# Optimization experiments

Measured on AMD Instinct MI355X. Metric: run time of the kernel, lower is better.

## Reference

```python
import jax, jax.numpy as jnp
import numpy as np

NEG_SLOPE = 0.2


def add_self_loops(edge_index, num_nodes):
    loop = jnp.arange(num_nodes, dtype=edge_index.dtype)
    return jnp.concatenate([edge_index, jnp.stack([loop, loop])], axis=1)


def gat_conv(x, edge_index, W, att_src, att_dst, bias, heads, out_ch, concat):
    # x: [N, F_in]; edge_index: [2, E]; W: [F_in, heads*out_ch]
    # att_src/att_dst: [heads, out_ch]; bias: [heads*out_ch] or [out_ch]
    N = x.shape[0]
    ei = add_self_loops(edge_index, N)
    src, dst = ei[0], ei[1]
    xw = (x @ W).reshape(N, heads, out_ch)          # [N, H, C]
    a_src = jnp.einsum('nhc,hc->nh', xw, att_src)    # [N, H]
    a_dst = jnp.einsum('nhc,hc->nh', xw, att_dst)    # [N, H]
    e = a_src[src] + a_dst[dst]                      # [E', H]
    e = jax.nn.leaky_relu(e, NEG_SLOPE)
    # segment softmax over edges grouped by destination node
    e_max = jax.ops.segment_max(e, dst, num_segments=N)  # [N, H]
    e_exp = jnp.exp(e - e_max[dst])
    denom = jax.ops.segment_sum(e_exp, dst, num_segments=N)  # [N, H]
    alpha = e_exp / denom[dst]                       # [E', H]
    msg = xw[src] * alpha[:, :, None]                # [E', H, C]
    out = jax.ops.segment_sum(msg, dst, num_segments=N)  # [N, H, C]
    if concat:
        out = out.reshape(N, heads * out_ch)
    else:
        out = out.mean(axis=1)
    return out + bias


def setup_inputs() -> dict:
    key = jax.random.key(0)
    ks = jax.random.split(key, 10)
    N, E = 100000, 1600000
    F_in, hid, heads, F_out = 128, 32, 4, 40
    s = 0.1
    x = jax.random.normal(ks[0], (N, F_in), dtype=jnp.float32)
    edge_index = jax.random.randint(ks[1], (2, E), 0, N, dtype=jnp.int64)
    W1 = jax.random.normal(ks[2], (F_in, heads * hid), dtype=jnp.float32) * s
    att_src1 = jax.random.normal(ks[3], (heads, hid), dtype=jnp.float32) * s
    att_dst1 = jax.random.normal(ks[4], (heads, hid), dtype=jnp.float32) * s
    b1 = jax.random.normal(ks[5], (heads * hid,), dtype=jnp.float32) * s
    W2 = jax.random.normal(ks[6], (heads * hid, F_out), dtype=jnp.float32) * s
    att_src2 = jax.random.normal(ks[7], (1, F_out), dtype=jnp.float32) * s
    att_dst2 = jax.random.normal(ks[8], (1, F_out), dtype=jnp.float32) * s
    b2 = jax.random.normal(ks[9], (F_out,), dtype=jnp.float32) * s
    return {"x": x, "edge_index": edge_index, "W1": W1, "att_src1": att_src1,
            "att_dst1": att_dst1, "b1": b1, "W2": W2, "att_src2": att_src2,
            "att_dst2": att_dst2, "b2": b2}


def reference(x, edge_index, W1, att_src1, att_dst1, b1, W2, att_src2, att_dst2, b2):
    h = gat_conv(x, edge_index, W1, att_src1, att_dst1, b1, heads=4, out_ch=32, concat=True)
    h = jax.nn.relu(h)
    out = gat_conv(h, edge_index, W2, att_src2, att_dst2, b2, heads=1, out_ch=40, concat=True)
    return out
```

## Files before the change

### kernel.cpp

```cpp
#include <hip/hip_runtime.h>
#include <hip/hip_bf16.h>

#define NEG_SLOPE 0.2f
#define LOG2E 1.4426950408889634f
#define HWREG_XCC_ID_FULL (((32 - 1) << 11) | (0 << 6) | 20)

typedef _Float16 f16;
typedef f16 f16x8 __attribute__((ext_vector_type(8)));
typedef float f32x4 __attribute__((ext_vector_type(4)));

__device__ __forceinline__ unsigned pack_h2(float a, float b) {
    union { f16 h[2]; unsigned u; } c;
    c.h[0] = (f16)a; c.h[1] = (f16)b;
    return c.u;
}

__device__ __forceinline__ void load_edge(const void* ei, int f64, int e, int E, int& s, int& d) {
    if (f64) {
        const long long* p = (const long long*)ei;
        s = (int)p[e];
        d = (int)p[(long long)E + e];
    } else {
        const int* p = (const int*)ei;
        s = p[e];
        d = p[E + e];
    }
}

__global__ void k_init(const int* __restrict__ ei32, int npairs, int* __restrict__ flag,
                       const float* __restrict__ W1, const float* __restrict__ W2,
                       f16* __restrict__ W1t, f16* __restrict__ W2t,
                       uint4* __restrict__ deg_part4, int nzero) {
    const int b = blockIdx.x, t = threadIdx.x;
    if (b == 0) {
        __shared__ int found;
        if (t == 0) found = 0;
        __syncthreads();
        for (int i = t; i < npairs; i += 256) {
            if (ei32[2 * i + 1] != 0) found = 1;
        }
        __syncthreads();
        if (t == 0) *flag = found ? 0 : 1;
    } else if (b <= 88) {
        int o = (b - 1) * 256 + t;
        if (o < 128 * 128) {
            int n = o >> 7, k = o & 127;
            W1t[o] = (f16)W1[k * 128 + n];
        } else {
            int o2 = o - 128 * 128;
            if (o2 < 48 * 128) {
                int n = o2 >> 7, k = o2 & 127;
                W2t[o2] = (f16)(n < 40 ? W2[k * 40 + n] : 0.f);
            }
        }
    } else {
        int idx = (b - 89) * 256 + t;
        if (idx < nzero) deg_part4[idx] = (uint4){0, 0, 0, 0};
    }
}

__global__ void k_degree(const void* __restrict__ ei, const int* __restrict__ flag,
                         int* __restrict__ deg_part, int* __restrict__ rank, int N, int E) {
    int e = blockIdx.x * blockDim.x + threadIdx.x;
    if (e >= E) return;
    int d;
    if (*flag) d = (int)((const long long*)ei)[(long long)E + e];
    else       d = ((const int*)ei)[E + e];
    int xcc = (int)(__builtin_amdgcn_s_getreg(HWREG_XCC_ID_FULL) & 7u);
    int lr = atomicAdd(&deg_part[xcc * N + d], 1);
    rank[e] = (xcc << 24) | lr;
}

__global__ __launch_bounds__(1024) void k_scan_blk(int* __restrict__ deg_part,
                                                   int* __restrict__ offsets,
                                                   int* __restrict__ blksum, int N) {
    __shared__ int wsums[16];
    const int t = threadIdx.x;
    const int lane = t & 63;
    const int wid = t >> 6;
    int idx = blockIdx.x * 4096 + t * 4;
    int v0 = 0, v1 = 0, v2 = 0, v3 = 0;
    if (((N & 3) == 0) && (idx + 3 < N)) {
        uint4 u[8];
#pragma unroll
        for (int x = 0; x < 8; x++) u[x] = *(uint4*)&deg_part[x * N + idx];
        int p0 = 0, p1 = 0, p2 = 0, p3 = 0;
#pragma unroll
        for (int x = 0; x < 8; x++) {
            uint4 w = u[x];
            u[x] = (uint4){(unsigned)p0, (unsigned)p1, (unsigned)p2, (unsigned)p3};
            p0 += (int)w.x; p1 += (int)w.y; p2 += (int)w.z; p3 += (int)w.w;
        }
#pragma unroll
        for (int x = 0; x < 8; x++) *(uint4*)&deg_part[x * N + idx] = u[x];
        v0 = p0; v1 = p1; v2 = p2; v3 = p3;
    } else if (idx < N) {
        int vv[4] = {0, 0, 0, 0};
        for (int i = 0; i < 4; i++) {
            int d = idx + i;
            if (d >= N) break;
            int p = 0;
#pragma unroll
            for (int x = 0; x < 8; x++) {
                int t0 = deg_part[x * N + d];
                deg_part[x * N + d] = p;
                p += t0;
            }
            vv[i] = p;
        }
        v0 = vv[0]; v1 = vv[1]; v2 = vv[2]; v3 = vv[3];
    }
    int s1 = v0 + v1, s2 = s1 + v2, s3 = s2 + v3;
    int inc = s3;
#pragma unroll
    for (int off = 1; off < 64; off <<= 1) {
        int y = __shfl_up(inc, off);
        if (lane >= off) inc += y;
    }
    if (lane == 63) wsums[wid] = inc;
    __syncthreads();
    if (wid == 0) {
        int v = (lane < 16) ? wsums[lane] : 0;
        int wi = v;
#pragma unroll
        for (int off = 1; off < 16; off <<= 1) {
            int y = __shfl_up(wi, off);
            if (lane >= off) wi += y;
        }
        if (lane < 16) wsums[lane] = wi - v;
        if (lane == 15) blksum[blockIdx.x] = wi;
    }
    __syncthreads();
    int excl = wsums[wid] + (inc - s3);
    if (idx + 0 < N) offsets[idx + 1] = excl + v0;
    if (idx + 1 < N) offsets[idx + 2] = excl + s1;
    if (idx + 2 < N) offsets[idx + 3] = excl + s2;
    if (idx + 3 < N) offsets[idx + 4] = excl + s3;
}

__global__ void k_scan_top(const int* __restrict__ blksum, int* __restrict__ blkoff, int G) {
    int l = threadIdx.x;
    int v = (l < G) ? blksum[l] : 0;
    int inc = v;
#pragma unroll
    for (int off = 1; off < 64; off <<= 1) {
        int y = __shfl_up(inc, off);
        if (l >= off) inc += y;
    }
    if (l < G) blkoff[l] = inc - v;
}

__global__ void k_scan_add(int* __restrict__ offsets, const int* __restrict__ blkoff, int N) {
    int n = blockIdx.x * blockDim.x + threadIdx.x;
    if (n >= N) return;
    offsets[n + 1] += blkoff[n >> 12];
    if (n == 0) offsets[0] = 0;
}

__global__ void k_scatter(const void* __restrict__ ei, const int* __restrict__ flag,
                          const int* __restrict__ offsets, const int* __restrict__ deg_part,
                          const int* __restrict__ rank, int* __restrict__ csr_src,
                          int N, int E) {
    int e = blockIdx.x * blockDim.x + threadIdx.x;
    if (e >= E) return;
    int s, d;
    load_edge(ei, *flag, e, E, s, d);
    int r = rank[e];
    int xcc = r >> 24;
    int lr = r & 0xFFFFFF;
    csr_src[offsets[d] + deg_part[xcc * N + d] + lr] = s;
}

__global__ __launch_bounds__(256) void k_gemm1(const float* __restrict__ X,
                                               const f16* __restrict__ W1t,
                                               const float* __restrict__ as1,
                                               const float* __restrict__ ad1,
                                               f16* __restrict__ Afh,
                                               float* __restrict__ aS1,
                                               float* __restrict__ aD1, int N) {
    __shared__ f16 sA[64 * 136];
    __shared__ f16 sB[128 * 136];
    const int t = threadIdx.x;
    const int row0 = blockIdx.x * 64;

    {
        int r = t >> 2, seg = t & 3;
        int row = row0 + r;
        if (row >= N) row = N - 1;
        const float4* xg = (const float4*)(X + (size_t)row * 128 + seg * 32);
        unsigned tmp[16];
#pragma unroll
        for (int j = 0; j < 8; j++) {
            float4 v = xg[j];
            tmp[2 * j]     = pack_h2(v.x, v.y);
            tmp[2 * j + 1] = pack_h2(v.z, v.w);
        }
        uint4* dst = (uint4*)&sA[r * 136 + seg * 32];
#pragma unroll
        for (int j = 0; j < 4; j++) dst[j] = ((uint4*)tmp)[j];
        int n = t >> 1, half = (t & 1) * 64;
        const uint4* src = (const uint4*)(W1t + n * 128 + half);
        uint4* dw = (uint4*)&sB[n * 136 + half];
#pragma unroll
        for (int j = 0; j < 8; j++) dw[j] = src[j];
    }
    __syncthreads();

    const int w = t >> 6, lane = t & 63, ln = lane & 15, q = lane >> 4;
    f32x4 acc[8];
#pragma unroll
    for (int c = 0; c < 8; c++) acc[c] = (f32x4){0.f, 0.f, 0.f, 0.f};

#pragma unroll
    for (int ks = 0; ks < 4; ks++) {
        f16x8 a = *(const f16x8*)&sA[(w * 16 + ln) * 136 + ks * 32 + q * 8];
#pragma unroll
        for (int c = 0; c < 8; c++) {
            f16x8 b = *(const f16x8*)&sB[(c * 16 + ln) * 136 + ks * 32 + q * 8];
            acc[c] = __builtin_amdgcn_mfma_f32_16x16x32_f16(a, b, acc[c], 0, 0, 0);
        }
    }

    const size_t H64 = (size_t)N * 64;
#pragma unroll
    for (int c = 0; c < 8; c++) {
        int half = c >> 2, cc = c & 3;
#pragma unroll
        for (int reg = 0; reg < 4; reg++) {
            int rg = row0 + w * 16 + q * 4 + reg;
            if (rg < N) Afh[half * H64 + (size_t)rg * 64 + cc * 16 + ln] = (f16)acc[c][reg];
        }
    }

    float ps[4][4], pd[4][4];
#pragma unroll
    for (int h = 0; h < 4; h++) {
        float as_lo = as1[32 * h + ln], as_hi = as1[32 * h + 16 + ln];
        float ad_lo = ad1[32 * h + ln], ad_hi = ad1[32 * h + 16 + ln];
#pragma unroll
        for (int reg = 0; reg < 4; reg++) {
            ps[h][reg] = acc[2 * h][reg] * as_lo + acc[2 * h + 1][reg] * as_hi;
            pd[h][reg] = acc[2 * h][reg] * ad_lo + acc[2 * h + 1][reg] * ad_hi;
        }
    }
#pragma unroll
    for (int h = 0; h < 4; h++)
#pragma unroll
        for (int reg = 0; reg < 4; reg++)
#pragma unroll
            for (int off = 1; off < 16; off <<= 1) {
                ps[h][reg] += __shfl_xor(ps[h][reg], off);
                pd[h][reg] += __shfl_xor(pd[h][reg], off);
            }
#pragma unroll
    for (int h = 0; h < 4; h++) {
        if (ln == 2 * h) {
#pragma unroll
            for (int reg = 0; reg < 4; reg++) {
                int rg = row0 + w * 16 + q * 4 + reg;
                if (rg < N) aS1[rg * 4 + h] = ps[h][reg] * LOG2E;
            }
        }
        if (ln == 2 * h + 1) {
#pragma unroll
            for (int reg = 0; reg < 4; reg++) {
                int rg = row0 + w * 16 + q * 4 + reg;
                if (rg < N) aD1[rg * 4 + h] = pd[h][reg] * LOG2E;
            }
        }
    }
}

__global__ __launch_bounds__(256) void k_gemm2(const f16* __restrict__ Hfh,
                                               const f16* __restrict__ W2t,
                                               const float* __restrict__ as2,
                                               const float* __restrict__ ad2,
                                               f16* __restrict__ X2f,
                                               float* __restrict__ aS2,
                                               float* __restrict__ aD2, int N) {
    __shared__ f16 sA[64 * 136];
    __shared__ f16 sB[48 * 136];
    const int t = threadIdx.x;
    const int row0 = blockIdx.x * 64;
    const size_t H64 = (size_t)N * 64;
    {
        int r = t >> 2, seg = t & 3;
        int row = row0 + r;
        if (row >= N) row = N - 1;
        const uint4* hg = (const uint4*)(Hfh + (size_t)(seg >> 1) * H64 +
                                         (size_t)row * 64 + (seg & 1) * 32);
        uint4* dst = (uint4*)&sA[r * 136 + seg * 32];
#pragma unroll
        for (int j = 0; j < 4; j++) dst[j] = hg[j];
        const uint4* wsrc = (const uint4*)W2t;
#pragma unroll
        for (int u = t; u < 768; u += 256) {
            int o = u * 8;
            int n = o >> 7, ko = o & 127;
            *(uint4*)&sB[n * 136 + ko] = wsrc[u];
        }
    }
    __syncthreads();

    const int w = t >> 6, lane = t & 63, ln = lane & 15, q = lane >> 4;
    f32x4 acc[3];
#pragma unroll
    for (int c = 0; c < 3; c++) acc[c] = (f32x4){0.f, 0.f, 0.f, 0.f};

#pragma unroll
    for (int ks = 0; ks < 4; ks++) {
        f16x8 a = *(const f16x8*)&sA[(w * 16 + ln) * 136 + ks * 32 + q * 8];
#pragma unroll
        for (int c = 0; c < 3; c++) {
            f16x8 b = *(const f16x8*)&sB[(c * 16 + ln) * 136 + ks * 32 + q * 8];
            acc[c] = __builtin_amdgcn_mfma_f32_16x16x32_f16(a, b, acc[c], 0, 0, 0);
        }
    }

#pragma unroll
    for (int c = 0; c < 3; c++) {
        int col = c * 16 + ln;
        if (col < 40) {
#pragma unroll
            for (int reg = 0; reg < 4; reg++) {
                int rg = row0 + w * 16 + q * 4 + reg;
                if (rg < N) X2f[(size_t)rg * 64 + col] = (f16)acc[c][reg];
            }
        }
    }

    float ps[4], pd[4];
#pragma unroll
    for (int reg = 0; reg < 4; reg++) { ps[reg] = 0.f; pd[reg] = 0.f; }
#pragma unroll
    for (int c = 0; c < 3; c++) {
        int col = c * 16 + ln;
        float as_ = (col < 40) ? as2[col] : 0.f;
        float ad_ = (col < 40) ? ad2[col] : 0.f;
#pragma unroll
        for (int reg = 0; reg < 4; reg++) {
            ps[reg] = fmaf(acc[c][reg], as_, ps[reg]);
            pd[reg] = fmaf(acc[c][reg], ad_, pd[reg]);
        }
    }
#pragma unroll
    for (int reg = 0; reg < 4; reg++) {
#pragma unroll
        for (int off = 1; off < 16; off <<= 1) {
            ps[reg] += __shfl_xor(ps[reg], off);
            pd[reg] += __shfl_xor(pd[reg], off);
        }
        int rg = row0 + w * 16 + q * 4 + reg;
        if (rg < N) {
            if (ln == 0) aS2[rg] = ps[reg] * LOG2E;
            if (ln == 1) aD2[rg] = pd[reg] * LOG2E;
        }
    }
}

__global__ __launch_bounds__(128) void k_msg1(const int* __restrict__ offsets,
                                              const int* __restrict__ csr_src,
                                              const float* __restrict__ aS,
                                              const float* __restrict__ aD,
                                              const f16* __restrict__ Afh,
                                              const float* __restrict__ b1,
                                              f16* __restrict__ Hfh, int N, int NB) {
    const int lane = threadIdx.x & 63;
    const int pass = (blockIdx.x >= NB) ? 1 : 0;
    const int blk = blockIdx.x - pass * NB;
    const int n = blk * 2 + (threadIdx.x >> 6);
    const bool node_ok = (n < N);
    const int g = lane >> 3;
    const int p = lane & 7;
    const int h = pass * 2 + (p >> 2);
    const size_t H64 = (size_t)N * 64;
    const f16* Af = Afh + (size_t)pass * H64;

    int b = 0, e = 0;
    float adh = 0.f;
    if (node_ok) {
        b = offsets[n];
        e = offsets[n + 1];
        adh = aD[n * 4 + h];
    }

    float acc[8];
#pragma unroll
    for (int k = 0; k < 8; k++) acc[k] = 0.f;
    float wsum = 0.f;

    if (node_ok) {
        float xs = aS[n * 4 + h] + adh;
        float ws = __builtin_amdgcn_exp2f(fmaxf(xs, NEG_SLOPE * xs));
        if (g != 0) ws = 0.f;
        const f16x8 hv = *(const f16x8*)(Af + (size_t)n * 64 + p * 8);
#pragma unroll
        for (int k = 0; k < 8; k++) acc[k] = fmaf(ws, (float)hv[k], acc[k]);
        wsum = ws;
    }

    int sreg = 0;
    if (node_ok && e > b) {
        int idx = b + lane;
        if (idx >= e) idx = e - 1;
        sreg = csr_src[idx];
    }

    int i = b;
#pragma unroll 2
    for (; i < e && (i - b) + 8 <= 64; i += 8) {
        int j = i + g;
        bool valid = (j < e);
        int s = __builtin_amdgcn_ds_bpermute((j - b) << 2, sreg);
        if (!valid) s = 0;
        float sv = aS[s * 4 + h];
        const f16x8 hv = *(const f16x8*)(Af + (size_t)s * 64 + p * 8);
        float x = sv + adh;
        float wgt = __builtin_amdgcn_exp2f(fmaxf(x, NEG_SLOPE * x));
        if (!valid) wgt = 0.f;
#pragma unroll
        for (int k = 0; k < 8; k++) acc[k] = fmaf(wgt, (float)hv[k], acc[k]);
        wsum += wgt;
    }
    for (; i < e; i += 8) {
        int j = i + g;
        bool valid = (j < e);
        int jc = valid ? j : (e - 1);
        int s = csr_src[jc];
        if (!valid) s = 0;
        float sv = aS[s * 4 + h];
        const f16x8 hv = *(const f16x8*)(Af + (size_t)s * 64 + p * 8);
        float x = sv + adh;
        float wgt = __builtin_amdgcn_exp2f(fmaxf(x, NEG_SLOPE * x));
        if (!valid) wgt = 0.f;
#pragma unroll
        for (int k = 0; k < 8; k++) acc[k] = fmaf(wgt, (float)hv[k], acc[k]);
        wsum += wgt;
    }

#pragma unroll
    for (int k = 0; k < 8; k++) {
        acc[k] += __shfl_xor(acc[k], 8);
        acc[k] += __shfl_xor(acc[k], 16);
        acc[k] += __shfl_xor(acc[k], 32);
    }
    wsum += __shfl_xor(wsum, 8);
    wsum += __shfl_xor(wsum, 16);
    wsum += __shfl_xor(wsum, 32);

    if (node_ok && g == 0) {
        float inv = __builtin_amdgcn_rcpf(wsum);
        const float4* bb = (const float4*)(b1 + pass * 64 + p * 8);
        float4 b0 = bb[0], b4 = bb[1];
        float bv[8] = {b0.x, b0.y, b0.z, b0.w, b4.x, b4.y, b4.z, b4.w};
        union { f16 h8[8]; uint4 u; } o;
#pragma unroll
        for (int k = 0; k < 8; k++) {
            float v = fmaf(acc[k], inv, bv[k]);
            o.h8[k] = (f16)fmaxf(v, 0.f);
        }
        *(uint4*)(Hfh + (size_t)pass * H64 + (size_t)n * 64 + p * 8) = o.u;
    }
}

__global__ __launch_bounds__(128) void k_msg2(const int* __restrict__ offsets,
                                              const int* __restrict__ csr_src,
                                              const float* __restrict__ aS,
                                              const float* __restrict__ aD,
                                              const f16* __restrict__ X2f,
                                              const float* __restrict__ b2,
                                              float* __restrict__ OUT, int N) {
    __shared__ float red[2][60][9];
    const int lane = threadIdx.x & 63;
    const int wv = threadIdx.x >> 6;
    const int n = blockIdx.x * 2 + wv;
    const bool node_ok = (n < N);
    const int g = lane / 5;
    const int p = lane % 5;
    const bool lane_ok = (g < 12);

    int b = 0, e = 0;
    float adh = 0.f;
    if (node_ok) {
        b = offsets[n];
        e = offsets[n + 1];
        adh = aD[n];
    }

    float acc[8];
#pragma unroll
    for (int k = 0; k < 8; k++) acc[k] = 0.f;
    float wsum = 0.f;

    if (node_ok) {
        float xs = aS[n] + adh;
        float ws = __builtin_amdgcn_exp2f(fmaxf(xs, NEG_SLOPE * xs));
        if (!(lane_ok && g == 0)) ws = 0.f;
        const f16x8 hv = *(const f16x8*)(X2f + (size_t)n * 64 + p * 8);
#pragma unroll
        for (int k = 0; k < 8; k++) acc[k] = fmaf(ws, (float)hv[k], acc[k]);
        wsum = ws;
    }

    int sreg = 0;
    if (node_ok && e > b) {
        int idx = b + lane;
        if (idx >= e) idx = e - 1;
        sreg = csr_src[idx];
    }

    int i = b;
    for (; i < e && (i - b) + 12 <= 64; i += 12) {
        int j = i + g;
        bool valid = lane_ok && (j < e);
        int s = __builtin_amdgcn_ds_bpermute(((j - b) & 63) << 2, sreg);
        if (!valid) s = 0;
        float sv = aS[s];
        const f16x8 hv = *(const f16x8*)(X2f + (size_t)s * 64 + p * 8);
        float x = sv + adh;
        float wgt = __builtin_amdgcn_exp2f(fmaxf(x, NEG_SLOPE * x));
        if (!valid) wgt = 0.f;
#pragma unroll
        for (int k = 0; k < 8; k++) acc[k] = fmaf(wgt, (float)hv[k], acc[k]);
        wsum += wgt;
    }
    for (; i < e; i += 12) {
        int j = i + g;
        bool valid = lane_ok && (j < e);
        int jc = (j < e) ? j : (e - 1);
        int s = csr_src[jc];
        if (!valid) s = 0;
        float sv = aS[s];
        const f16x8 hv = *(const f16x8*)(X2f + (size_t)s * 64 + p * 8);
        float x = sv + adh;
        float wgt = __builtin_amdgcn_exp2f(fmaxf(x, NEG_SLOPE * x));
        if (!valid) wgt = 0.f;
#pragma unroll
        for (int k = 0; k < 8; k++) acc[k] = fmaf(wgt, (float)hv[k], acc[k]);
        wsum += wgt;
    }

    if (lane_ok) {
#pragma unroll
        for (int k = 0; k < 8; k++) red[wv][lane][k] = acc[k];
        red[wv][lane][8] = wsum;
    }
    __syncthreads();

    if (node_ok && lane < 40) {
        int pp = lane >> 3, kk = lane & 7;
        float s_ = 0.f, ws_ = 0.f;
#pragma unroll
        for (int gg = 0; gg < 12; gg++) {
            s_  += red[wv][gg * 5 + pp][kk];
            ws_ += red[wv][gg * 5][8];
        }
        float inv = __builtin_amdgcn_rcpf(ws_);
        OUT[(size_t)n * 40 + lane] = fmaf(s_, inv, b2[lane]);
    }
}

extern "C" void kernel_launch(void* const* d_in, const int* in_sizes, int n_in,
                              void* d_out, int out_size, void* d_ws, size_t ws_size,
                              hipStream_t stream) {
    const float* x   = (const float*)d_in[0];
    const void*  ei  = d_in[1];
    const float* W1  = (const float*)d_in[2];
    const float* as1 = (const float*)d_in[3];
    const float* ad1 = (const float*)d_in[4];
    const float* b1  = (const float*)d_in[5];
    const float* W2  = (const float*)d_in[6];
    const float* as2 = (const float*)d_in[7];
    const float* ad2 = (const float*)d_in[8];
    const float* b2  = (const float*)d_in[9];
    float* out = (float*)d_out;

    const int N = in_sizes[0] / 128;
    const int E = in_sizes[1] / 2;

    char* w = (char*)d_ws;
    auto alloc = [&](size_t bytes) {
        char* p = w;
        w += (bytes + 15) & ~(size_t)15;
        return p;
    };
    int* flag      = (int*)alloc(16);
    int* offsets   = (int*)alloc((size_t)(N + 1) * 4);
    int* deg_part  = (int*)alloc((size_t)N * 8 * 4);
    int* rank      = (int*)alloc((size_t)E * 4);
    int* csr_src   = (int*)alloc((size_t)E * 4);
    int* blksum    = (int*)alloc(64 * 4);
    int* blkoff    = (int*)alloc(64 * 4);
    float* aS1     = (float*)alloc((size_t)N * 4 * 4);
    float* aD1     = (float*)alloc((size_t)N * 4 * 4);
    float* aS2     = (float*)alloc((size_t)N * 4);
    float* aD2     = (float*)alloc((size_t)N * 4);
    f16* W1t       = (f16*)alloc(128 * 128 * 2);
    f16* W2t       = (f16*)alloc(48 * 128 * 2);
    f16* Afh       = (f16*)alloc((size_t)N * 128 * 2);
    f16* X2f       = (f16*)alloc((size_t)N * 64 * 2);
    f16* Hfh       = (f16*)alloc((size_t)N * 128 * 2);

    const int nzero = 2 * N;
    k_init<<<89 + (nzero + 255) / 256, 256, 0, stream>>>(
        (const int*)ei, 1024, flag, W1, W2, W1t, W2t, (uint4*)deg_part, nzero);

    k_degree<<<(E + 255) / 256, 256, 0, stream>>>(ei, flag, deg_part, rank, N, E);
    const int G = (N + 4095) / 4096;
    k_scan_blk<<<G, 1024, 0, stream>>>(deg_part, offsets, blksum, N);
    k_scan_top<<<1, 64, 0, stream>>>(blksum, blkoff, G);
    k_scan_add<<<(N + 255) / 256, 256, 0, stream>>>(offsets, blkoff, N);
    k_scatter<<<(E + 255) / 256, 256, 0, stream>>>(ei, flag, offsets, deg_part, rank,
                                                   csr_src, N, E);

    const int gb = (N + 63) / 64;
    k_gemm1<<<gb, 256, 0, stream>>>(x, W1t, as1, ad1, Afh, aS1, aD1, N);
    const int NB = (N + 1) / 2;
    k_msg1<<<2 * NB, 128, 0, stream>>>(offsets, csr_src, aS1, aD1, Afh, b1, Hfh, N, NB);

    k_gemm2<<<gb, 256, 0, stream>>>(Hfh, W2t, as2, ad2, X2f, aS2, aD2, N);
    k_msg2<<<(N + 1) / 2, 128, 0, stream>>>(offsets, csr_src, aS2, aD2, X2f, b2, out, N);
}
```

Baseline: 405.3 us.

## Merge split-head layer-1 layout into one pass, add nontemporal loads and stores

Layer-1 features were stored as two half-head planes, and the layer-1 aggregation ran as two passes over the edges. They are now stored as one 128-wide row per node and aggregated in a single pass: 16 lanes cover a row, and each wave handles 4 edges per step instead of 8. This halves the CSR index and attention traversal for layer 1 but doubles the gather width per edge. Nontemporal load and store hints are also added across many streaming accesses, and the message kernels now use 4 waves (256 threads) per block instead of 2. Marking accesses as nontemporal risks evicting data from cache that is later reused, such as Af and Hf, which are read again by the next kernel.

After: 431.4 us. +6.4%, slower.

```diff
diff --git a/kernel.cpp b/kernel.cpp
--- a/kernel.cpp
+++ b/kernel.cpp
@@ -8,23 +8,31 @@
 typedef _Float16 f16;
 typedef f16 f16x8 __attribute__((ext_vector_type(8)));
 typedef float f32x4 __attribute__((ext_vector_type(4)));
+typedef float fvec4 __attribute__((ext_vector_type(4)));
+typedef unsigned uvec4 __attribute__((ext_vector_type(4)));
+
+template <typename T>
+__device__ __forceinline__ T ntload(const T* p) { return __builtin_nontemporal_load(p); }
+template <typename T>
+__device__ __forceinline__ void ntstore(T* p, T v) { __builtin_nontemporal_store(v, p); }
+
+__device__ __forceinline__ float4 ntload4f(const float4* p) {
+    fvec4 v = __builtin_nontemporal_load((const fvec4*)p);
+    return make_float4(v.x, v.y, v.z, v.w);
+}
+__device__ __forceinline__ uint4 ntload4u(const uint4* p) {
+    uvec4 v = __builtin_nontemporal_load((const uvec4*)p);
+    return (uint4){v.x, v.y, v.z, v.w};
+}
+__device__ __forceinline__ void ntstore4u(uint4* p, uint4 v) {
+    uvec4 t = {v.x, v.y, v.z, v.w};
+    __builtin_nontemporal_store(t, (uvec4*)p);
+}
 
 __device__ __forceinline__ unsigned pack_h2(float a, float b) {
     union { f16 h[2]; unsigned u; } c;
     c.h[0] = (f16)a; c.h[1] = (f16)b;
     return c.u;
-}
-
-__device__ __forceinline__ void load_edge(const void* ei, int f64, int e, int E, int& s, int& d) {
-    if (f64) {
-        const long long* p = (const long long*)ei;
-        s = (int)p[e];
-        d = (int)p[(long long)E + e];
-    } else {
-        const int* p = (const int*)ei;
-        s = p[e];
-        d = p[E + e];
-    }
 }
 
 __global__ void k_init(const int* __restrict__ ei32, int npairs, int* __restrict__ flag,
@@ -64,11 +72,11 @@
     int e = blockIdx.x * blockDim.x + threadIdx.x;
     if (e >= E) return;
     int d;
-    if (*flag) d = (int)((const long long*)ei)[(long long)E + e];
-    else       d = ((const int*)ei)[E + e];
+    if (*flag) d = (int)ntload(&((const long long*)ei)[(long long)E + e]);
+    else       d = ntload(&((const int*)ei)[E + e]);
     int xcc = (int)(__builtin_amdgcn_s_getreg(HWREG_XCC_ID_FULL) & 7u);
     int lr = atomicAdd(&deg_part[xcc * N + d], 1);
-    rank[e] = (xcc << 24) | lr;
+    ntstore(&rank[e], (xcc << 24) | lr);
 }
 
 __global__ __launch_bounds__(1024) void k_scan_blk(int* __restrict__ deg_part,
@@ -164,18 +172,26 @@
     int e = blockIdx.x * blockDim.x + threadIdx.x;
     if (e >= E) return;
     int s, d;
-    load_edge(ei, *flag, e, E, s, d);
-    int r = rank[e];
+    if (*flag) {
+        const long long* p = (const long long*)ei;
+        s = (int)ntload(&p[e]);
+        d = (int)ntload(&p[(long long)E + e]);
+    } else {
+        const int* p = (const int*)ei;
+        s = ntload(&p[e]);
+        d = ntload(&p[E + e]);
+    }
+    int r = ntload(&rank[e]);
     int xcc = r >> 24;
     int lr = r & 0xFFFFFF;
-    csr_src[offsets[d] + deg_part[xcc * N + d] + lr] = s;
+    ntstore(&csr_src[offsets[d] + deg_part[xcc * N + d] + lr], s);
 }
 
 __global__ __launch_bounds__(256) void k_gemm1(const float* __restrict__ X,
                                                const f16* __restrict__ W1t,
                                                const float* __restrict__ as1,
                                                const float* __restrict__ ad1,
-                                               f16* __restrict__ Afh,
+                                               f16* __restrict__ Af,
                                                float* __restrict__ aS1,
                                                float* __restrict__ aD1, int N) {
     __shared__ f16 sA[64 * 136];
@@ -191,7 +207,7 @@
         unsigned tmp[16];
 #pragma unroll
         for (int j = 0; j < 8; j++) {
-            float4 v = xg[j];
+            float4 v = ntload4f(&xg[j]);
             tmp[2 * j]     = pack_h2(v.x, v.y);
             tmp[2 * j + 1] = pack_h2(v.z, v.w);
         }
@@ -221,16 +237,13 @@
         }
     }
 
-    const size_t H64 = (size_t)N * 64;
-#pragma unroll
-    for (int c = 0; c < 8; c++) {
-        int half = c >> 2, cc = c & 3;
+#pragma unroll
+    for (int c = 0; c < 8; c++)
 #pragma unroll
         for (int reg = 0; reg < 4; reg++) {
             int rg = row0 + w * 16 + q * 4 + reg;
-            if (rg < N) Afh[half * H64 + (size_t)rg * 64 + cc * 16 + ln] = (f16)acc[c][reg];
-        }
-    }
+            if (rg < N) ntstore(&Af[(size_t)rg * 128 + c * 16 + ln], (f16)acc[c][reg]);
+        }
 
     float ps[4][4], pd[4][4];
 #pragma unroll
@@ -271,7 +284,7 @@
     }
 }
 
-__global__ __launch_bounds__(256) void k_gemm2(const f16* __restrict__ Hfh,
+__global__ __launch_bounds__(256) void k_gemm2(const f16* __restrict__ Hf,
                                                const f16* __restrict__ W2t,
                                                const float* __restrict__ as2,
                                                const float* __restrict__ ad2,
@@ -282,16 +295,14 @@
     __shared__ f16 sB[48 * 136];
     const int t = threadIdx.x;
     const int row0 = blockIdx.x * 64;
-    const size_t H64 = (size_t)N * 64;
     {
         int r = t >> 2, seg = t & 3;
         int row = row0 + r;
         if (row >= N) row = N - 1;
-        const uint4* hg = (const uint4*)(Hfh + (size_t)(seg >> 1) * H64 +
-                                         (size_t)row * 64 + (seg & 1) * 32);
+        const uint4* hg = (const uint4*)(Hf + (size_t)row * 128 + seg * 32);
         uint4* dst = (uint4*)&sA[r * 136 + seg * 32];
 #pragma unroll
-        for (int j = 0; j < 4; j++) dst[j] = hg[j];
+        for (int j = 0; j < 4; j++) dst[j] = ntload4u(&hg[j]);
         const uint4* wsrc = (const uint4*)W2t;
 #pragma unroll
         for (int u = t; u < 768; u += 256) {
@@ -358,23 +369,19 @@
     }
 }
 
-__global__ __launch_bounds__(128) void k_msg1(const int* __restrict__ offsets,
+__global__ __launch_bounds__(256) void k_msg1(const int* __restrict__ offsets,
                                               const int* __restrict__ csr_src,
                                               const float* __restrict__ aS,
                                               const float* __restrict__ aD,
-                                              const f16* __restrict__ Afh,
+                                              const f16* __restrict__ Af,
                                               const float* __restrict__ b1,
-                                              f16* __restrict__ Hfh, int N, int NB) {
+                                              f16* __restrict__ Hf, int N) {
     const int lane = threadIdx.x & 63;
-    const int pass = (blockIdx.x >= NB) ? 1 : 0;
-    const int blk = blockIdx.x - pass * NB;
-    const int n = blk * 2 + (threadIdx.x >> 6);
+    const int n = blockIdx.x * 4 + (threadIdx.x >> 6);
     const bool node_ok = (n < N);
-    const int g = lane >> 3;
-    const int p = lane & 7;
-    const int h = pass * 2 + (p >> 2);
-    const size_t H64 = (size_t)N * 64;
-    const f16* Af = Afh + (size_t)pass * H64;
+    const int g = lane >> 4;
+    const int p = lane & 15;
+    const int h = p >> 2;
 
     int b = 0, e = 0;
     float adh = 0.f;
@@ -393,7 +400,7 @@
         float xs = aS[n * 4 + h] + adh;
         float ws = __builtin_amdgcn_exp2f(fmaxf(xs, NEG_SLOPE * xs));
         if (g != 0) ws = 0.f;
-        const f16x8 hv = *(const f16x8*)(Af + (size_t)n * 64 + p * 8);
+        const f16x8 hv = *(const f16x8*)(Af + (size_t)n * 128 + p * 8);
 #pragma unroll
         for (int k = 0; k < 8; k++) acc[k] = fmaf(ws, (float)hv[k], acc[k]);
         wsum = ws;
@@ -403,18 +410,18 @@
     if (node_ok && e > b) {
         int idx = b + lane;
         if (idx >= e) idx = e - 1;
-        sreg = csr_src[idx];
+        sreg = ntload(&csr_src[idx]);
     }
 
     int i = b;
 #pragma unroll 2
-    for (; i < e && (i - b) + 8 <= 64; i += 8) {
+    for (; i < e && (i - b) + 4 <= 64; i += 4) {
         int j = i + g;
         bool valid = (j < e);
         int s = __builtin_amdgcn_ds_bpermute((j - b) << 2, sreg);
         if (!valid) s = 0;
         float sv = aS[s * 4 + h];
-        const f16x8 hv = *(const f16x8*)(Af + (size_t)s * 64 + p * 8);
+        const f16x8 hv = *(const f16x8*)(Af + (size_t)s * 128 + p * 8);
         float x = sv + adh;
         float wgt = __builtin_amdgcn_exp2f(fmaxf(x, NEG_SLOPE * x));
         if (!valid) wgt = 0.f;
@@ -422,14 +429,14 @@
         for (int k = 0; k < 8; k++) acc[k] = fmaf(wgt, (float)hv[k], acc[k]);
         wsum += wgt;
     }
-    for (; i < e; i += 8) {
+    for (; i < e; i += 4) {
         int j = i + g;
         bool valid = (j < e);
         int jc = valid ? j : (e - 1);
         int s = csr_src[jc];
         if (!valid) s = 0;
         float sv = aS[s * 4 + h];
-        const f16x8 hv = *(const f16x8*)(Af + (size_t)s * 64 + p * 8);
+        const f16x8 hv = *(const f16x8*)(Af + (size_t)s * 128 + p * 8);
         float x = sv + adh;
         float wgt = __builtin_amdgcn_exp2f(fmaxf(x, NEG_SLOPE * x));
         if (!valid) wgt = 0.f;
@@ -440,17 +447,15 @@
 
 #pragma unroll
     for (int k = 0; k < 8; k++) {
-        acc[k] += __shfl_xor(acc[k], 8);
         acc[k] += __shfl_xor(acc[k], 16);
         acc[k] += __shfl_xor(acc[k], 32);
     }
-    wsum += __shfl_xor(wsum, 8);
     wsum += __shfl_xor(wsum, 16);
     wsum += __shfl_xor(wsum, 32);
 
     if (node_ok && g == 0) {
         float inv = __builtin_amdgcn_rcpf(wsum);
-        const float4* bb = (const float4*)(b1 + pass * 64 + p * 8);
+        const float4* bb = (const float4*)(b1 + p * 8);
         float4 b0 = bb[0], b4 = bb[1];
         float bv[8] = {b0.x, b0.y, b0.z, b0.w, b4.x, b4.y, b4.z, b4.w};
         union { f16 h8[8]; uint4 u; } o;
@@ -459,21 +464,21 @@
             float v = fmaf(acc[k], inv, bv[k]);
             o.h8[k] = (f16)fmaxf(v, 0.f);
         }
-        *(uint4*)(Hfh + (size_t)pass * H64 + (size_t)n * 64 + p * 8) = o.u;
-    }
-}
-
-__global__ __launch_bounds__(128) void k_msg2(const int* __restrict__ offsets,
+        ntstore4u((uint4*)(Hf + (size_t)n * 128 + p * 8), o.u);
+    }
+}
+
+__global__ __launch_bounds__(256) void k_msg2(const int* __restrict__ offsets,
                                               const int* __restrict__ csr_src,
                                               const float* __restrict__ aS,
                                               const float* __restrict__ aD,
                                               const f16* __restrict__ X2f,
                                               const float* __restrict__ b2,
                                               float* __restrict__ OUT, int N) {
-    __shared__ float red[2][60][9];
+    __shared__ float red[4][60][9];
     const int lane = threadIdx.x & 63;
     const int wv = threadIdx.x >> 6;
-    const int n = blockIdx.x * 2 + wv;
+    const int n = blockIdx.x * 4 + wv;
     const bool node_ok = (n < N);
     const int g = lane / 5;
     const int p = lane % 5;
@@ -506,7 +511,7 @@
     if (node_ok && e > b) {
         int idx = b + lane;
         if (idx >= e) idx = e - 1;
-        sreg = csr_src[idx];
+        sreg = ntload(&csr_src[idx]);
     }
 
     int i = b;
@@ -556,7 +561,7 @@
             ws_ += red[wv][gg * 5][8];
         }
         float inv = __builtin_amdgcn_rcpf(ws_);
-        OUT[(size_t)n * 40 + lane] = fmaf(s_, inv, b2[lane]);
+        ntstore(&OUT[(size_t)n * 40 + lane], fmaf(s_, inv, b2[lane]));
     }
 }
 
@@ -597,9 +602,9 @@
     float* aD2     = (float*)alloc((size_t)N * 4);
     f16* W1t       = (f16*)alloc(128 * 128 * 2);
     f16* W2t       = (f16*)alloc(48 * 128 * 2);
-    f16* Afh       = (f16*)alloc((size_t)N * 128 * 2);
+    f16* Af        = (f16*)alloc((size_t)N * 128 * 2);
     f16* X2f       = (f16*)alloc((size_t)N * 64 * 2);
-    f16* Hfh       = (f16*)alloc((size_t)N * 128 * 2);
+    f16* Hf        = (f16*)alloc((size_t)N * 128 * 2);
 
     const int nzero = 2 * N;
     k_init<<<89 + (nzero + 255) / 256, 256, 0, stream>>>(
@@ -614,10 +619,9 @@
                                                    csr_src, N, E);
 
     const int gb = (N + 63) / 64;
-    k_gemm1<<<gb, 256, 0, stream>>>(x, W1t, as1, ad1, Afh, aS1, aD1, N);
-    const int NB = (N + 1) / 2;
-    k_msg1<<<2 * NB, 128, 0, stream>>>(offsets, csr_src, aS1, aD1, Afh, b1, Hfh, N, NB);
-
-    k_gemm2<<<gb, 256, 0, stream>>>(Hfh, W2t, as2, ad2, X2f, aS2, aD2, N);
-    k_msg2<<<(N + 1) / 2, 128, 0, stream>>>(offsets, csr_src, aS2, aD2, X2f, b2, out, N);
-}
+    k_gemm1<<<gb, 256, 0, stream>>>(x, W1t, as1, ad1, Af, aS1, aD1, N);
+    k_msg1<<<(N + 3) / 4, 256, 0, stream>>>(offsets, csr_src, aS1, aD1, Af, b1, Hf, N);
+
+    k_gemm2<<<gb, 256, 0, stream>>>(Hf, W2t, as2, ad2, X2f, aS2, aD2, N);
+    k_msg2<<<(N + 3) / 4, 256, 0, stream>>>(offsets, csr_src, aS2, aD2, X2f, b2, out, N);
+}
```
